# Kernel tuning notes

Measured on AMD Instinct MI355X. Metric: run time of the kernel, lower is better.

The kernel has to match this reference:

```python
import jax, jax.numpy as jnp
import numpy as np

B, N, D = 8, 1024, 768
H = 12
HD = D // H
LN_EPS = 1e-5
EPS = 1e-8


def setup_inputs() -> dict:
    key = jax.random.key(0)
    ks = jax.random.split(key, 16)
    s = 0.02
    return {
        "x": jax.random.normal(ks[0], (B, N, D), jnp.float32),
        "low_freq_feat": jax.random.normal(ks[1], (B, N, D), jnp.float32),
        "high_freq_feat": jax.random.normal(ks[2], (B, N, D), jnp.float32),
        "W_qkv_id": jax.random.normal(ks[3], (D, 3 * D), jnp.float32) * s,
        "W_qkv_attr": jax.random.normal(ks[4], (D, 3 * D), jnp.float32) * s,
        "W_fg_id": jax.random.normal(ks[5], (D, D), jnp.float32) * s,
        "b_fg_id": jnp.zeros((D,), jnp.float32),
        "W_fg_attr": jax.random.normal(ks[6], (D, D), jnp.float32) * s,
        "b_fg_attr": jnp.zeros((D,), jnp.float32),
        "W_proj_id": jax.random.normal(ks[7], (D, D), jnp.float32) * s,
        "b_proj_id": jnp.zeros((D,), jnp.float32),
        "W_proj_attr": jax.random.normal(ks[8], (D, D), jnp.float32) * s,
        "b_proj_attr": jnp.zeros((D,), jnp.float32),
        "ln_id_g": jnp.ones((D,), jnp.float32),
        "ln_id_b": jnp.zeros((D,), jnp.float32),
        "ln_attr_g": jnp.ones((D,), jnp.float32),
        "ln_attr_b": jnp.zeros((D,), jnp.float32),
        "ortho_temperature": jnp.float32(1.0),
        "freq_guide_strength": jnp.float32(0.3),
    }


def _layernorm(x, g, b):
    mu = x.mean(-1, keepdims=True)
    var = ((x - mu) ** 2).mean(-1, keepdims=True)
    return (x - mu) * jax.lax.rsqrt(var + LN_EPS) * g + b


def reference(x, low_freq_feat, high_freq_feat,
              W_qkv_id, W_qkv_attr,
              W_fg_id, b_fg_id, W_fg_attr, b_fg_attr,
              W_proj_id, b_proj_id, W_proj_attr, b_proj_attr,
              ln_id_g, ln_id_b, ln_attr_g, ln_attr_b,
              ortho_temperature, freq_guide_strength):
    b, n, d = x.shape
    scale = HD ** -0.5

    def split_qkv(t):
        t = t.reshape(b, n, 3, H, HD).transpose(2, 0, 3, 1, 4)
        return t[0], t[1], t[2]

    q_id, k_id, v_id = split_qkv(x @ W_qkv_id)
    q_at, k_at, v_at = split_qkv(x @ W_qkv_attr)

    fs = jax.nn.sigmoid(freq_guide_strength)
    low_g = (low_freq_feat @ W_fg_id + b_fg_id).reshape(b, n, H, HD).transpose(0, 2, 1, 3)
    high_g = (high_freq_feat @ W_fg_attr + b_fg_attr).reshape(b, n, H, HD).transpose(0, 2, 1, 3)
    v_id = v_id + fs * low_g
    v_at = v_at + fs * high_g

    def soft_attn(q, k):
        a = jnp.clip(jnp.einsum('bhnd,bhmd->bhnm', q, k) * scale, -20.0, 20.0)
        return jax.nn.softmax(a, axis=-1)

    attn_id = soft_attn(q_id, k_id)
    attn_at = soft_attn(q_at, k_at)

    # soft orthogonal mask (same mask for both branches)
    overlap = ((attn_id + EPS) * (attn_at + EPS)).sum(-1, keepdims=True)
    temp = jnp.clip(ortho_temperature, 0.1, 5.0)
    mask = jax.nn.sigmoid(-overlap * temp)

    def mask_renorm(a):
        m = a * mask
        m = m / (m.sum(-1, keepdims=True) + EPS)
        return jnp.where(jnp.isnan(m), jnp.zeros_like(m), m)

    attn_id = mask_renorm(attn_id)
    attn_at = mask_renorm(attn_at)

    def branch_out(a, v, W, bias, g, beta):
        o = jnp.einsum('bhnm,bhmd->bhnd', a, v).transpose(0, 2, 1, 3).reshape(b, n, d)
        return _layernorm(o @ W + bias, g, beta)

    id_features = branch_out(attn_id, v_id, W_proj_id, b_proj_id, ln_id_g, ln_id_b)
    attr_features = branch_out(attn_at, v_at, W_proj_attr, b_proj_attr, ln_attr_g, ln_attr_b)
    return (id_features, attr_features)
```

## Files before the change

kernel.cpp:

```cpp
#include <hip/hip_runtime.h>
#include <stdint.h>


typedef __attribute__((ext_vector_type(8))) _Float16 f16x8;
typedef __attribute__((ext_vector_type(4))) _Float16 f16x4;
typedef __attribute__((ext_vector_type(4))) float    f32x4;

__device__ __forceinline__ void g2l16(const void* g, void* l) {
  __builtin_amdgcn_global_load_lds(
      (const __attribute__((address_space(1))) void*)g,
      (__attribute__((address_space(3))) void*)l, 16, 0, 0);
}

#define BARX()   asm volatile("s_barrier" ::: "memory")
#define WAITV(N) asm volatile("s_waitcnt vmcnt(" #N ")" ::: "memory")

template <bool SWAP>
__device__ __forceinline__ void gemm256(const _Float16* __restrict__ A,
                                        const _Float16* __restrict__ Bt,
                                        int K, int m0, int n0,
                                        _Float16* As, _Float16* Bs,
                                        f32x4 (&acc)[8][4]) {
  const int tid = threadIdx.x;
  const int lane = tid & 63, w = tid >> 6;
  const int wm = (w >> 2) * 128, wn = (w & 3) * 64;
  const int l15 = lane & 15, quad = lane >> 4;
  const int srow = lane >> 2;
  const int scol = ((lane & 3) ^ ((lane >> 3) & 3)) * 8;
  const int rg = (quad ^ ((l15 >> 1) & 3)) * 8;
  const int c0 = w * 2, c1 = c0 + 1;
  const _Float16* pA0 = A + (m0 + c0 * 16 + srow) * K + scol;
  const _Float16* pA1 = A + (m0 + c1 * 16 + srow) * K + scol;
  const _Float16* pB0 = Bt + (n0 + c0 * 16 + srow) * K + scol;
  const _Float16* pB1 = Bt + (n0 + c1 * 16 + srow) * K + scol;

#pragma unroll
  for (int mt = 0; mt < 8; mt++)
#pragma unroll
    for (int nt = 0; nt < 4; nt++) acc[mt][nt] = (f32x4){0.f, 0.f, 0.f, 0.f};

  const int KT = K >> 5;

#pragma unroll
  for (int t = 0; t < 3; t++) {
    int kc = t * 32, bj = t * 8192;
    g2l16(pA0 + kc, As + bj + c0 * 512);
    g2l16(pB0 + kc, Bs + bj + c0 * 512);
    g2l16(pA1 + kc, As + bj + c1 * 512);
    g2l16(pB1 + kc, Bs + bj + c1 * 512);
  }
  WAITV(8);
  BARX();

  auto tile = [&](int t, bool doStage) {
    const int bj = (t & 3) * 8192;
    const _Float16* as = As + bj;
    const _Float16* bs = Bs + bj;
    const int kcn = (t + 3) * 32;
    const int bn = ((t + 3) & 3) * 8192;
    f16x8 a[8];
#pragma unroll
    for (int mt = 0; mt < 8; mt++)
      a[mt] = *(const f16x8*)(as + (wm + mt * 16 + l15) * 32 + rg);
    f16x8 b0 = *(const f16x8*)(bs + (wn + l15) * 32 + rg);
    f16x8 b1 = *(const f16x8*)(bs + (wn + 16 + l15) * 32 + rg);
    if (doStage) {
      g2l16(pA0 + kcn, As + bn + c0 * 512);
      g2l16(pA1 + kcn, As + bn + c1 * 512);
    }
    __builtin_amdgcn_s_setprio(1);
#pragma unroll
    for (int mt = 0; mt < 8; mt++) {
      acc[mt][0] = SWAP
          ? __builtin_amdgcn_mfma_f32_16x16x32_f16(b0, a[mt], acc[mt][0], 0, 0, 0)
          : __builtin_amdgcn_mfma_f32_16x16x32_f16(a[mt], b0, acc[mt][0], 0, 0, 0);
      acc[mt][1] = SWAP
          ? __builtin_amdgcn_mfma_f32_16x16x32_f16(b1, a[mt], acc[mt][1], 0, 0, 0)
          : __builtin_amdgcn_mfma_f32_16x16x32_f16(a[mt], b1, acc[mt][1], 0, 0, 0);
    }
    __builtin_amdgcn_s_setprio(0);
    BARX();
    f16x8 b2 = *(const f16x8*)(bs + (wn + 32 + l15) * 32 + rg);
    f16x8 b3 = *(const f16x8*)(bs + (wn + 48 + l15) * 32 + rg);
    if (doStage) {
      g2l16(pB0 + kcn, Bs + bn + c0 * 512);
      g2l16(pB1 + kcn, Bs + bn + c1 * 512);
    }
    __builtin_amdgcn_s_setprio(1);
#pragma unroll
    for (int mt = 0; mt < 8; mt++) {
      acc[mt][2] = SWAP
          ? __builtin_amdgcn_mfma_f32_16x16x32_f16(b2, a[mt], acc[mt][2], 0, 0, 0)
          : __builtin_amdgcn_mfma_f32_16x16x32_f16(a[mt], b2, acc[mt][2], 0, 0, 0);
      acc[mt][3] = SWAP
          ? __builtin_amdgcn_mfma_f32_16x16x32_f16(b3, a[mt], acc[mt][3], 0, 0, 0)
          : __builtin_amdgcn_mfma_f32_16x16x32_f16(a[mt], b3, acc[mt][3], 0, 0, 0);
    }
    __builtin_amdgcn_s_setprio(0);
  };

  int t = 0;
  for (; t < KT - 3; ++t) {
    tile(t, true);
    WAITV(8);
    BARX();
  }
  tile(t, false); WAITV(4); BARX(); ++t;
  tile(t, false); WAITV(0); BARX(); ++t;
  tile(t, false);
}

__global__ __launch_bounds__(256) void k_cast3(const float* __restrict__ s0,
                                               const float* __restrict__ s1,
                                               const float* __restrict__ s2,
                                               _Float16* __restrict__ d0,
                                               _Float16* __restrict__ d1,
                                               _Float16* __restrict__ d2) {
  int blk = blockIdx.x;
  const float* s; _Float16* d;
  if (blk < 6144)       { s = s0; d = d0; }
  else if (blk < 12288) { s = s1; d = d1; blk -= 6144; }
  else                  { s = s2; d = d2; blk -= 12288; }
  int i = blk * 256 + threadIdx.x;
  float4 v = ((const float4*)s)[i];
  f16x4 o = {(_Float16)v.x, (_Float16)v.y, (_Float16)v.z, (_Float16)v.w};
  *(f16x4*)(d + (size_t)i * 4) = o;
}

__device__ __forceinline__ void tcast32(const float* __restrict__ src,
                                        _Float16* __restrict__ dst,
                                        int N, int n0, int k0) {
  __shared__ float t[32][33];
  int tr = threadIdx.x >> 5, tc = threadIdx.x & 31;
#pragma unroll
  for (int i = 0; i < 4; i++) {
    int r = tr + i * 8;
    t[r][tc] = src[(size_t)(k0 + r) * N + n0 + tc];
  }
  __syncthreads();
#pragma unroll
  for (int i = 0; i < 4; i++) {
    int r = tr + i * 8;
    dst[(size_t)(n0 + r) * 768 + k0 + tc] = (_Float16)t[tc][r];
  }
}

__global__ __launch_bounds__(256) void k_tcast_all(const float* __restrict__ Wq0,
                                                   const float* __restrict__ Wq1,
                                                   const float* __restrict__ W0,
                                                   const float* __restrict__ W1,
                                                   const float* __restrict__ W2,
                                                   const float* __restrict__ W3,
                                                   _Float16* __restrict__ Dq,
                                                   _Float16* __restrict__ D0,
                                                   _Float16* __restrict__ D1,
                                                   _Float16* __restrict__ D2,
                                                   _Float16* __restrict__ D3) {
  int blk = blockIdx.x;
  if (blk < 3456) {
    int half = blk / 1728, rem = blk % 1728;
    int xx = rem % 72, yy = rem / 72;
    tcast32(half ? Wq1 : Wq0, Dq + (size_t)half * 2304 * 768, 2304, xx * 32, yy * 32);
  } else {
    blk -= 3456;
    int q = blk / 576, rem = blk % 576;
    int xx = rem % 24, yy = rem / 24;
    const float* src; _Float16* d;
    if (q == 0)      { src = W0; d = D0; }
    else if (q == 1) { src = W1; d = D1; }
    else if (q == 2) { src = W2; d = D2; }
    else             { src = W3; d = D3; }
    tcast32(src, d, 768, xx * 32, yy * 32);
  }
}

__global__ __launch_bounds__(512, 2) void k_gemm_qkv(const _Float16* __restrict__ A,
                                                     const _Float16* __restrict__ Bt,
                                                     _Float16* __restrict__ Qb,
                                                     _Float16* __restrict__ Kb,
                                                     _Float16* __restrict__ Vtb) {
  __shared__ alignas(16) _Float16 As[32768], Bs[32768];
  f32x4 acc[8][4];
  int m0 = blockIdx.y * 256, n0 = blockIdx.x * 256;
  int br = n0 / 2304;
  int three = (n0 - br * 2304) / 768;
  int lane = threadIdx.x & 63, w = threadIdx.x >> 6;
  int wm = (w >> 2) * 128, wn = (w & 3) * 64, l15 = lane & 15, quad = lane >> 4;

  if (three == 2) {
    gemm256<false>(A, Bt, 768, m0, n0, As, Bs, acc);
#pragma unroll
    for (int mt = 0; mt < 8; mt++)
#pragma unroll
      for (int nt = 0; nt < 4; nt++) {
        int n = n0 + wn + nt * 16 + l15;
        int c = n - br * 2304 - 1536;
        int h = c >> 6, hd = c & 63;
        int m = m0 + wm + mt * 16 + quad * 4;
        int b = m >> 10, tok = m & 1023;
        size_t head = (size_t)(br * 96 + b * 12 + h);
        f32x4 v = acc[mt][nt];
        f16x4 o;
#pragma unroll
        for (int r = 0; r < 4; r++) o[r] = (_Float16)v[r];
        *(f16x4*)(Vtb + (head * 64 + hd) * 1024 + tok) = o;
      }
  } else {
    gemm256<true>(A, Bt, 768, m0, n0, As, Bs, acc);
    float qscl = (three == 0) ? 0.125f * 1.44269504f : 1.0f;
    _Float16* dst = (three == 0) ? Qb : Kb;
#pragma unroll
    for (int mt = 0; mt < 8; mt++)
#pragma unroll
      for (int nt = 0; nt < 4; nt++) {
        int m = m0 + wm + mt * 16 + l15;
        int n = n0 + wn + nt * 16 + quad * 4;
        int c = n - br * 2304 - three * 768;
        int h = c >> 6, hd = c & 63;
        int b = m >> 10, tok = m & 1023;
        size_t head = (size_t)(br * 96 + b * 12 + h);
        f32x4 v = acc[mt][nt];
        f16x4 o;
#pragma unroll
        for (int r = 0; r < 4; r++) o[r] = (_Float16)(v[r] * qscl);
        *(f16x4*)(dst + (head * 1024 + tok) * 64 + hd) = o;
      }
  }
}

__global__ __launch_bounds__(512, 2) void k_gemm_fgadd(const _Float16* __restrict__ Alo,
                                                       const _Float16* __restrict__ Ahi,
                                                       const _Float16* __restrict__ Bid,
                                                       const _Float16* __restrict__ Bat,
                                                       const float* __restrict__ bid,
                                                       const float* __restrict__ bat,
                                                       const float* __restrict__ fgs,
                                                       _Float16* __restrict__ Vtb) {
  __shared__ alignas(16) _Float16 As[32768], Bs[32768];
  f32x4 acc[8][4];
  int br = blockIdx.x / 3;
  int n0 = (blockIdx.x % 3) * 256, m0 = blockIdx.y * 256;
  const _Float16* A = br ? Ahi : Alo;
  const _Float16* Bt = br ? Bat : Bid;
  const float* bias = br ? bat : bid;
  gemm256<false>(A, Bt, 768, m0, n0, As, Bs, acc);
  float fs = 1.f / (1.f + __expf(-fgs[0]));
  int lane = threadIdx.x & 63, w = threadIdx.x >> 6;
  int wm = (w >> 2) * 128, wn = (w & 3) * 64, l15 = lane & 15, quad = lane >> 4;
#pragma unroll
  for (int mt = 0; mt < 8; mt++)
#pragma unroll
    for (int nt = 0; nt < 4; nt++) {
      int c = n0 + wn + nt * 16 + l15;
      int h = c >> 6, hd = c & 63;
      int m = m0 + wm + mt * 16 + quad * 4;
      int b = m >> 10, tok = m & 1023;
      size_t head = (size_t)(br * 96 + b * 12 + h);
      float bv = bias[c];
      f32x4 v = acc[mt][nt];
      _Float16* p = Vtb + (head * 64 + hd) * 1024 + tok;
      f16x4 old = *(const f16x4*)p;
      f16x4 o;
#pragma unroll
      for (int r = 0; r < 4; r++)
        o[r] = (_Float16)((float)old[r] + fs * (v[r] + bv));
      *(f16x4*)p = o;
    }
}

__global__ __launch_bounds__(256, 3) void k_attn(const _Float16* __restrict__ Qb,
                                                 const _Float16* __restrict__ Kb,
                                                 const _Float16* __restrict__ Vtb,
                                                 _Float16* __restrict__ Ob) {
  __shared__ alignas(16) _Float16 Qs[128 * 64];
  __shared__ alignas(16) _Float16 Ks[128 * 64];
  __shared__ alignas(16) _Float16 Vts[64 * 128];
  int hl = blockIdx.x;
  int br = hl / 96, bh = hl % 96;
  int qbase = blockIdx.y * 128;
  const _Float16* Qh = Qb + (size_t)hl * 65536;
  const _Float16* Kh = Kb + (size_t)hl * 65536;
  const _Float16* Vth = Vtb + (size_t)hl * 65536;
  int lane = threadIdx.x & 63, w = threadIdx.x >> 6;
  int l15 = lane & 15, quad = lane >> 4;
  const int key7 = l15 & 7;

  {
    int rr = lane >> 3, sg = (lane & 7) ^ rr;
#pragma unroll
    for (int i = 0; i < 4; i++) {
      int c = w * 4 + i;
      g2l16(Qh + (size_t)(qbase + c * 8 + rr) * 64 + sg * 8, Qs + c * 512);
    }
  }
  auto stage_kv = [&](int n0) {
    int rr8 = lane >> 3, sg8 = ((lane & 7) ^ rr8) * 8;
    int rr16 = lane >> 4;
#pragma unroll
    for (int i = 0; i < 4; i++) {
      int c = w * 4 + i;
      g2l16(Kh + (size_t)(n0 + c * 8 + rr8) * 64 + sg8, Ks + c * 512);
      int vrow = c * 4 + rr16;
      int sg16 = ((lane & 15) ^ (vrow & 15)) * 8;
      g2l16(Vth + (size_t)vrow * 1024 + n0 + sg16, Vts + c * 512);
    }
  };
  stage_kv(0);

  f32x4 o[2][4];
#pragma unroll
  for (int qg = 0; qg < 2; qg++)
#pragma unroll
    for (int i = 0; i < 4; i++) o[qg][i] = (f32x4){0.f, 0.f, 0.f, 0.f};
  float rs0 = 0.f, rs1 = 0.f;
  f16x8 bq[2][2];
  const f32x4 zero = (f32x4){0.f, 0.f, 0.f, 0.f};
  const int g0 = (quad ^ key7) * 8, g1 = ((4 + quad) ^ key7) * 8;

  for (int kt = 0; kt < 8; kt++) {
    __syncthreads();
    if (kt == 0) {
#pragma unroll
      for (int qg = 0; qg < 2; qg++) {
        bq[qg][0] = *(const f16x8*)(Qs + (w * 32 + qg * 16 + l15) * 64 + g0);
        bq[qg][1] = *(const f16x8*)(Qs + (w * 32 + qg * 16 + l15) * 64 + g1);
      }
    }
    f32x4 c0, c1;
    {
      f16x8 a0 = *(const f16x8*)(Ks + l15 * 64 + g0);
      f16x8 a1 = *(const f16x8*)(Ks + l15 * 64 + g1);
      c0 = __builtin_amdgcn_mfma_f32_16x16x32_f16(a0, bq[0][0], zero, 0, 0, 0);
      c0 = __builtin_amdgcn_mfma_f32_16x16x32_f16(a1, bq[0][1], c0, 0, 0, 0);
      c1 = __builtin_amdgcn_mfma_f32_16x16x32_f16(a0, bq[1][0], zero, 0, 0, 0);
      c1 = __builtin_amdgcn_mfma_f32_16x16x32_f16(a1, bq[1][1], c1, 0, 0, 0);
    }
#pragma unroll
    for (int nt = 0; nt < 8; nt++) {
      f32x4 n0_, n1_;
      if (nt < 7) {
        f16x8 a0 = *(const f16x8*)(Ks + ((nt + 1) * 16 + l15) * 64 + g0);
        f16x8 a1 = *(const f16x8*)(Ks + ((nt + 1) * 16 + l15) * 64 + g1);
        n0_ = __builtin_amdgcn_mfma_f32_16x16x32_f16(a0, bq[0][0], zero, 0, 0, 0);
        n0_ = __builtin_amdgcn_mfma_f32_16x16x32_f16(a1, bq[0][1], n0_, 0, 0, 0);
        n1_ = __builtin_amdgcn_mfma_f32_16x16x32_f16(a0, bq[1][0], zero, 0, 0, 0);
        n1_ = __builtin_amdgcn_mfma_f32_16x16x32_f16(a1, bq[1][1], n1_, 0, 0, 0);
      }
      f16x4 pt0, pt1;
#pragma unroll
      for (int r = 0; r < 4; r++) {
        float p = __builtin_amdgcn_exp2f(c0[r]);
        rs0 += p; pt0[r] = (_Float16)p;
      }
#pragma unroll
      for (int r = 0; r < 4; r++) {
        float p = __builtin_amdgcn_exp2f(c1[r]);
        rs1 += p; pt1[r] = (_Float16)p;
      }
#pragma unroll
      for (int hdt = 0; hdt < 4; hdt++) {
        int g = ((2 * nt + (quad >> 1)) ^ l15) * 8 + (quad & 1) * 4;
        f16x4 av = *(const f16x4*)(Vts + (hdt * 16 + l15) * 128 + g);
        o[0][hdt] = __builtin_amdgcn_mfma_f32_16x16x16f16(av, pt0, o[0][hdt], 0, 0, 0);
        o[1][hdt] = __builtin_amdgcn_mfma_f32_16x16x16f16(av, pt1, o[1][hdt], 0, 0, 0);
      }
      if (nt < 7) { c0 = n0_; c1 = n1_; }
    }
    __syncthreads();
    if (kt < 7) stage_kv((kt + 1) * 128);
  }
  int b = bh / 12, h = bh % 12;
#pragma unroll
  for (int qg = 0; qg < 2; qg++) {
    float l = qg ? rs1 : rs0;
    l += __shfl_xor(l, 16);
    l += __shfl_xor(l, 32);
    float inv = 1.f / l;
    size_t rowb = ((size_t)br * 8192 + b * 1024 + qbase + w * 32 + qg * 16 + l15) * 768 +
                  h * 64;
#pragma unroll
    for (int hdt = 0; hdt < 4; hdt++) {
      f16x4 u;
#pragma unroll
      for (int r = 0; r < 4; r++) u[r] = (_Float16)(o[qg][hdt][r] * inv);
      *(f16x4*)(Ob + rowb + hdt * 16 + quad * 4) = u;
    }
  }
}

__global__ __launch_bounds__(512, 2) void k_gemm_proj2(const _Float16* __restrict__ Aid,
                                                       const _Float16* __restrict__ Aat,
                                                       const _Float16* __restrict__ Bid,
                                                       const _Float16* __restrict__ Bat,
                                                       _Float16* __restrict__ Yid,
                                                       _Float16* __restrict__ Yat) {
  __shared__ alignas(16) _Float16 As[32768], Bs[32768];
  f32x4 acc[8][4];
  int half = blockIdx.x / 3;
  int n0 = (blockIdx.x % 3) * 256, m0 = blockIdx.y * 256;
  const _Float16* A = half ? Aat : Aid;
  const _Float16* Bt = half ? Bat : Bid;
  _Float16* Y = half ? Yat : Yid;
  gemm256<true>(A, Bt, 768, m0, n0, As, Bs, acc);
  int lane = threadIdx.x & 63, w = threadIdx.x >> 6;
  int wm = (w >> 2) * 128, wn = (w & 3) * 64, l15 = lane & 15, quad = lane >> 4;
#pragma unroll
  for (int mt = 0; mt < 8; mt++)
#pragma unroll
    for (int nt = 0; nt < 4; nt++) {
      int m = m0 + wm + mt * 16 + l15;
      int n = n0 + wn + nt * 16 + quad * 4;
      f32x4 v = acc[mt][nt];
      f16x4 o;
#pragma unroll
      for (int r = 0; r < 4; r++) o[r] = (_Float16)v[r];
      *(f16x4*)(Y + (size_t)m * 768 + n) = o;
    }
}

__global__ __launch_bounds__(256) void k_ln(const _Float16* __restrict__ Yid,
                                            const _Float16* __restrict__ Yat,
                                            const float* __restrict__ bp_id,
                                            const float* __restrict__ bp_at,
                                            const float* __restrict__ g_id,
                                            const float* __restrict__ be_id,
                                            const float* __restrict__ g_at,
                                            const float* __restrict__ be_at,
                                            float* __restrict__ out) {
  int w = threadIdx.x >> 6, lane = threadIdx.x & 63;
  int r = blockIdx.x * 4 + w;
  int br = r >> 13, m = r & 8191;
  const _Float16* Y = br ? Yat : Yid;
  const float* bp = br ? bp_at : bp_id;
  const float* g = br ? g_at : g_id;
  const float* be = br ? be_at : be_id;
  float v[12], sum = 0.f, sq = 0.f;
#pragma unroll
  for (int j = 0; j < 3; j++) {
    int c = j * 256 + lane * 4;
    f16x4 y = *(const f16x4*)(Y + (size_t)m * 768 + c);
    float4 bv = *(const float4*)(bp + c);
#pragma unroll
    for (int r2 = 0; r2 < 4; r2++) {
      float t = (float)y[r2] + ((const float*)&bv)[r2];
      v[j * 4 + r2] = t; sum += t; sq += t * t;
    }
  }
#pragma unroll
  for (int d = 1; d < 64; d <<= 1) { sum += __shfl_xor(sum, d); sq += __shfl_xor(sq, d); }
  float mu = sum * (1.f / 768.f);
  float var = sq * (1.f / 768.f) - mu * mu;
  float rstd = rsqrtf(var + 1e-5f);
  float* op = out + (size_t)br * 6291456 + (size_t)m * 768;
#pragma unroll
  for (int j = 0; j < 3; j++) {
    int c = j * 256 + lane * 4;
    float4 gv = *(const float4*)(g + c);
    float4 bev = *(const float4*)(be + c);
    float4 ov;
#pragma unroll
    for (int r2 = 0; r2 < 4; r2++)
      ((float*)&ov)[r2] = (v[j * 4 + r2] - mu) * rstd * ((const float*)&gv)[r2] +
                          ((const float*)&bev)[r2];
    *(float4*)(op + c) = ov;
  }
}

extern "C" void kernel_launch(void* const* d_in, const int* in_sizes, int n_in,
                              void* d_out, int out_size, void* d_ws, size_t ws_size,
                              hipStream_t stream) {
  const float* x       = (const float*)d_in[0];
  const float* lowf    = (const float*)d_in[1];
  const float* highf   = (const float*)d_in[2];
  const float* Wqkv_id = (const float*)d_in[3];
  const float* Wqkv_at = (const float*)d_in[4];
  const float* Wfg_id  = (const float*)d_in[5];
  const float* bfg_id  = (const float*)d_in[6];
  const float* Wfg_at  = (const float*)d_in[7];
  const float* bfg_at  = (const float*)d_in[8];
  const float* Wpr_id  = (const float*)d_in[9];
  const float* bpr_id  = (const float*)d_in[10];
  const float* Wpr_at  = (const float*)d_in[11];
  const float* bpr_at  = (const float*)d_in[12];
  const float* g_id    = (const float*)d_in[13];
  const float* be_id   = (const float*)d_in[14];
  const float* g_at    = (const float*)d_in[15];
  const float* be_at   = (const float*)d_in[16];
  const float* fgs     = (const float*)d_in[18];

  char* ws = (char*)d_ws;
  _Float16* x_f    = (_Float16*)(ws + 0);
  _Float16* low_f  = (_Float16*)(ws + 12582912);
  _Float16* high_f = (_Float16*)(ws + 25165824);
  _Float16* wqkvt  = (_Float16*)(ws + 37748736);
  _Float16* wfgidt = (_Float16*)(ws + 44826624);
  _Float16* wfgatt = (_Float16*)(ws + 46006272);
  _Float16* wpridt = (_Float16*)(ws + 47185920);
  _Float16* wpratt = (_Float16*)(ws + 48365568);
  _Float16* Qb     = (_Float16*)(ws + 74711040);
  _Float16* Kb     = (_Float16*)(ws + 99876864);
  _Float16* Vtb    = (_Float16*)(ws + 125042688);
  _Float16* Ob     = (_Float16*)(ws + 150208512);
  _Float16* Y_id   = (_Float16*)(ws + 0);
  _Float16* Y_at   = (_Float16*)(ws + 49545216);

  k_cast3<<<18432, 256, 0, stream>>>(x, lowf, highf, x_f, low_f, high_f);
  k_tcast_all<<<5760, 256, 0, stream>>>(Wqkv_id, Wqkv_at, Wfg_id, Wfg_at, Wpr_id, Wpr_at,
                                        wqkvt, wfgidt, wfgatt, wpridt, wpratt);
  k_gemm_qkv<<<dim3(18, 32), 512, 0, stream>>>(x_f, wqkvt, Qb, Kb, Vtb);
  k_gemm_fgadd<<<dim3(6, 32), 512, 0, stream>>>(low_f, high_f, wfgidt, wfgatt,
                                                bfg_id, bfg_at, fgs, Vtb);
  k_attn<<<dim3(192, 8), 256, 0, stream>>>(Qb, Kb, Vtb, Ob);
  k_gemm_proj2<<<dim3(6, 32), 512, 0, stream>>>(Ob, Ob + 6291456, wpridt, wpratt,
                                                Y_id, Y_at);
  k_ln<<<4096, 256, 0, stream>>>(Y_id, Y_at, bpr_id, bpr_at, g_id, be_id, g_at, be_at,
                                 (float*)d_out);
}
```

Before: 410.3 us.

## Reshape GEMM warp tiling to 64x128 per wave with explicit barrier scheduling

Changes the per-wave output tile in the shared 256x256 GEMM from 128x64 to 64x128, so each wave loads 4 A fragments and 8 B fragments per k-step instead of 8 and 4. The main loop is rewritten as a single loop with explicit barriers, lgkmcnt waits and sched_barriers between the two MFMA halves. The goal is to balance LDS reads and control instruction interleaving in the QKV, frequency-guide and projection GEMMs. The extra barriers per k-step add synchronization cost, and the epilogues are updated to the new accumulator layout.

```diff
diff --git a/kernel.cpp b/kernel.cpp
--- a/kernel.cpp
+++ b/kernel.cpp
@@ -14,100 +14,95 @@
 
 #define BARX()   asm volatile("s_barrier" ::: "memory")
 #define WAITV(N) asm volatile("s_waitcnt vmcnt(" #N ")" ::: "memory")
+#define LGKM0()  asm volatile("s_waitcnt lgkmcnt(0)" ::: "memory")
+#define SB0()    __builtin_amdgcn_sched_barrier(0)
+
+#define MFMA16(NB)                                                             \
+  __builtin_amdgcn_s_setprio(1);                                               \
+  _Pragma("unroll")                                                            \
+  for (int mt = 0; mt < 4; mt++)                                               \
+    _Pragma("unroll")                                                          \
+    for (int i = 0; i < 4; i++)                                                \
+      acc[mt][(NB) + i] = SWAP                                                 \
+          ? __builtin_amdgcn_mfma_f32_16x16x32_f16(b[(NB) + i], a[mt],         \
+                                                   acc[mt][(NB) + i], 0, 0, 0) \
+          : __builtin_amdgcn_mfma_f32_16x16x32_f16(a[mt], b[(NB) + i],         \
+                                                   acc[mt][(NB) + i], 0, 0, 0);\
+  __builtin_amdgcn_s_setprio(0);
 
 template <bool SWAP>
 __device__ __forceinline__ void gemm256(const _Float16* __restrict__ A,
                                         const _Float16* __restrict__ Bt,
                                         int K, int m0, int n0,
                                         _Float16* As, _Float16* Bs,
-                                        f32x4 (&acc)[8][4]) {
+                                        f32x4 (&acc)[4][8]) {
   const int tid = threadIdx.x;
   const int lane = tid & 63, w = tid >> 6;
-  const int wm = (w >> 2) * 128, wn = (w & 3) * 64;
+  const int wm = (w >> 1) * 64, wn = (w & 1) * 128;
   const int l15 = lane & 15, quad = lane >> 4;
   const int srow = lane >> 2;
   const int scol = ((lane & 3) ^ ((lane >> 3) & 3)) * 8;
   const int rg = (quad ^ ((l15 >> 1) & 3)) * 8;
-  const int c0 = w * 2, c1 = c0 + 1;
-  const _Float16* pA0 = A + (m0 + c0 * 16 + srow) * K + scol;
-  const _Float16* pA1 = A + (m0 + c1 * 16 + srow) * K + scol;
-  const _Float16* pB0 = Bt + (n0 + c0 * 16 + srow) * K + scol;
-  const _Float16* pB1 = Bt + (n0 + c1 * 16 + srow) * K + scol;
-
-#pragma unroll
-  for (int mt = 0; mt < 8; mt++)
-#pragma unroll
-    for (int nt = 0; nt < 4; nt++) acc[mt][nt] = (f32x4){0.f, 0.f, 0.f, 0.f};
-
+  const int rdA = (wm + l15) * 32 + rg;
+  const int rdB = (wn + l15) * 32 + rg;
   const int KT = K >> 5;
 
-#pragma unroll
-  for (int t = 0; t < 3; t++) {
-    int kc = t * 32, bj = t * 8192;
-    g2l16(pA0 + kc, As + bj + c0 * 512);
-    g2l16(pB0 + kc, Bs + bj + c0 * 512);
-    g2l16(pA1 + kc, As + bj + c1 * 512);
-    g2l16(pB1 + kc, Bs + bj + c1 * 512);
-  }
+  const _Float16* gA0 = A + (size_t)(m0 + (w * 2) * 16 + srow) * K + scol;
+  const _Float16* gA1 = gA0 + (size_t)16 * K;
+  const _Float16* gB0 = Bt + (size_t)(n0 + (w * 2) * 16 + srow) * K + scol;
+  const _Float16* gB1 = gB0 + (size_t)16 * K;
+
+  auto stageA = [&](int t) {
+    _Float16* Ab = As + (t & 3) * 8192 + w * 1024;
+    const int kc = t * 32;
+    g2l16(gA0 + kc, Ab);
+    g2l16(gA1 + kc, Ab + 512);
+  };
+  auto stageB = [&](int t) {
+    _Float16* Bb = Bs + (t & 3) * 8192 + w * 1024;
+    const int kc = t * 32;
+    g2l16(gB0 + kc, Bb);
+    g2l16(gB1 + kc, Bb + 512);
+  };
+
+#pragma unroll
+  for (int mt = 0; mt < 4; mt++)
+#pragma unroll
+    for (int nt = 0; nt < 8; nt++) acc[mt][nt] = (f32x4){0.f, 0.f, 0.f, 0.f};
+
+  stageA(0); stageB(0);
+  stageA(1); stageB(1);
+  stageA(2); stageB(2);
   WAITV(8);
   BARX();
 
-  auto tile = [&](int t, bool doStage) {
-    const int bj = (t & 3) * 8192;
-    const _Float16* as = As + bj;
-    const _Float16* bs = Bs + bj;
-    const int kcn = (t + 3) * 32;
-    const int bn = ((t + 3) & 3) * 8192;
-    f16x8 a[8];
-#pragma unroll
-    for (int mt = 0; mt < 8; mt++)
-      a[mt] = *(const f16x8*)(as + (wm + mt * 16 + l15) * 32 + rg);
-    f16x8 b0 = *(const f16x8*)(bs + (wn + l15) * 32 + rg);
-    f16x8 b1 = *(const f16x8*)(bs + (wn + 16 + l15) * 32 + rg);
-    if (doStage) {
-      g2l16(pA0 + kcn, As + bn + c0 * 512);
-      g2l16(pA1 + kcn, As + bn + c1 * 512);
-    }
-    __builtin_amdgcn_s_setprio(1);
-#pragma unroll
-    for (int mt = 0; mt < 8; mt++) {
-      acc[mt][0] = SWAP
-          ? __builtin_amdgcn_mfma_f32_16x16x32_f16(b0, a[mt], acc[mt][0], 0, 0, 0)
-          : __builtin_amdgcn_mfma_f32_16x16x32_f16(a[mt], b0, acc[mt][0], 0, 0, 0);
-      acc[mt][1] = SWAP
-          ? __builtin_amdgcn_mfma_f32_16x16x32_f16(b1, a[mt], acc[mt][1], 0, 0, 0)
-          : __builtin_amdgcn_mfma_f32_16x16x32_f16(a[mt], b1, acc[mt][1], 0, 0, 0);
-    }
-    __builtin_amdgcn_s_setprio(0);
+  for (int t = 0; t < KT; t++) {
+    const _Float16* as = As + (t & 3) * 8192;
+    const _Float16* bs = Bs + (t & 3) * 8192;
+    const bool st = (t + 3 < KT);
+    f16x8 a[4], b[8];
+
+#pragma unroll
+    for (int mt = 0; mt < 4; mt++) a[mt] = *(const f16x8*)(as + rdA + mt * 512);
+#pragma unroll
+    for (int i = 0; i < 4; i++) b[i] = *(const f16x8*)(bs + rdB + i * 512);
+    if (st) stageA(t + 3);
+    BARX(); LGKM0(); SB0();
+    MFMA16(0);
+    SB0();
     BARX();
-    f16x8 b2 = *(const f16x8*)(bs + (wn + 32 + l15) * 32 + rg);
-    f16x8 b3 = *(const f16x8*)(bs + (wn + 48 + l15) * 32 + rg);
-    if (doStage) {
-      g2l16(pB0 + kcn, Bs + bn + c0 * 512);
-      g2l16(pB1 + kcn, Bs + bn + c1 * 512);
-    }
-    __builtin_amdgcn_s_setprio(1);
-#pragma unroll
-    for (int mt = 0; mt < 8; mt++) {
-      acc[mt][2] = SWAP
-          ? __builtin_amdgcn_mfma_f32_16x16x32_f16(b2, a[mt], acc[mt][2], 0, 0, 0)
-          : __builtin_amdgcn_mfma_f32_16x16x32_f16(a[mt], b2, acc[mt][2], 0, 0, 0);
-      acc[mt][3] = SWAP
-          ? __builtin_amdgcn_mfma_f32_16x16x32_f16(b3, a[mt], acc[mt][3], 0, 0, 0)
-          : __builtin_amdgcn_mfma_f32_16x16x32_f16(a[mt], b3, acc[mt][3], 0, 0, 0);
-    }
-    __builtin_amdgcn_s_setprio(0);
-  };
-
-  int t = 0;
-  for (; t < KT - 3; ++t) {
-    tile(t, true);
-    WAITV(8);
-    BARX();
-  }
-  tile(t, false); WAITV(4); BARX(); ++t;
-  tile(t, false); WAITV(0); BARX(); ++t;
-  tile(t, false);
+
+#pragma unroll
+    for (int i = 4; i < 8; i++) b[i] = *(const f16x8*)(bs + rdB + i * 512);
+    if (st) stageB(t + 3);
+    BARX(); LGKM0(); SB0();
+    MFMA16(4);
+    SB0();
+    if (t + 3 < KT)      { WAITV(8); }
+    else if (t + 2 < KT) { WAITV(4); }
+    else if (t + 1 < KT) { WAITV(0); }
+    if (t + 1 < KT) BARX();
+  }
 }
 
 __global__ __launch_bounds__(256) void k_cast3(const float* __restrict__ s0,
@@ -180,19 +175,19 @@
                                                      _Float16* __restrict__ Kb,
                                                      _Float16* __restrict__ Vtb) {
   __shared__ alignas(16) _Float16 As[32768], Bs[32768];
-  f32x4 acc[8][4];
+  f32x4 acc[4][8];
   int m0 = blockIdx.y * 256, n0 = blockIdx.x * 256;
   int br = n0 / 2304;
   int three = (n0 - br * 2304) / 768;
   int lane = threadIdx.x & 63, w = threadIdx.x >> 6;
-  int wm = (w >> 2) * 128, wn = (w & 3) * 64, l15 = lane & 15, quad = lane >> 4;
+  int wm = (w >> 1) * 64, wn = (w & 1) * 128, l15 = lane & 15, quad = lane >> 4;
 
   if (three == 2) {
     gemm256<false>(A, Bt, 768, m0, n0, As, Bs, acc);
 #pragma unroll
-    for (int mt = 0; mt < 8; mt++)
-#pragma unroll
-      for (int nt = 0; nt < 4; nt++) {
+    for (int mt = 0; mt < 4; mt++)
+#pragma unroll
+      for (int nt = 0; nt < 8; nt++) {
         int n = n0 + wn + nt * 16 + l15;
         int c = n - br * 2304 - 1536;
         int h = c >> 6, hd = c & 63;
@@ -210,9 +205,9 @@
     float qscl = (three == 0) ? 0.125f * 1.44269504f : 1.0f;
     _Float16* dst = (three == 0) ? Qb : Kb;
 #pragma unroll
-    for (int mt = 0; mt < 8; mt++)
-#pragma unroll
-      for (int nt = 0; nt < 4; nt++) {
+    for (int mt = 0; mt < 4; mt++)
+#pragma unroll
+      for (int nt = 0; nt < 8; nt++) {
         int m = m0 + wm + mt * 16 + l15;
         int n = n0 + wn + nt * 16 + quad * 4;
         int c = n - br * 2304 - three * 768;
@@ -237,7 +232,7 @@
                                                        const float* __restrict__ fgs,
                                                        _Float16* __restrict__ Vtb) {
   __shared__ alignas(16) _Float16 As[32768], Bs[32768];
-  f32x4 acc[8][4];
+  f32x4 acc[4][8];
   int br = blockIdx.x / 3;
   int n0 = (blockIdx.x % 3) * 256, m0 = blockIdx.y * 256;
   const _Float16* A = br ? Ahi : Alo;
@@ -246,11 +241,11 @@
   gemm256<false>(A, Bt, 768, m0, n0, As, Bs, acc);
   float fs = 1.f / (1.f + __expf(-fgs[0]));
   int lane = threadIdx.x & 63, w = threadIdx.x >> 6;
-  int wm = (w >> 2) * 128, wn = (w & 3) * 64, l15 = lane & 15, quad = lane >> 4;
-#pragma unroll
-  for (int mt = 0; mt < 8; mt++)
-#pragma unroll
-    for (int nt = 0; nt < 4; nt++) {
+  int wm = (w >> 1) * 64, wn = (w & 1) * 128, l15 = lane & 15, quad = lane >> 4;
+#pragma unroll
+  for (int mt = 0; mt < 4; mt++)
+#pragma unroll
+    for (int nt = 0; nt < 8; nt++) {
       int c = n0 + wn + nt * 16 + l15;
       int h = c >> 6, hd = c & 63;
       int m = m0 + wm + mt * 16 + quad * 4;
@@ -395,7 +390,7 @@
                                                        _Float16* __restrict__ Yid,
                                                        _Float16* __restrict__ Yat) {
   __shared__ alignas(16) _Float16 As[32768], Bs[32768];
-  f32x4 acc[8][4];
+  f32x4 acc[4][8];
   int half = blockIdx.x / 3;
   int n0 = (blockIdx.x % 3) * 256, m0 = blockIdx.y * 256;
   const _Float16* A = half ? Aat : Aid;
@@ -403,11 +398,11 @@
   _Float16* Y = half ? Yat : Yid;
   gemm256<true>(A, Bt, 768, m0, n0, As, Bs, acc);
   int lane = threadIdx.x & 63, w = threadIdx.x >> 6;
-  int wm = (w >> 2) * 128, wn = (w & 3) * 64, l15 = lane & 15, quad = lane >> 4;
-#pragma unroll
-  for (int mt = 0; mt < 8; mt++)
-#pragma unroll
-    for (int nt = 0; nt < 4; nt++) {
+  int wm = (w >> 1) * 64, wn = (w & 1) * 128, l15 = lane & 15, quad = lane >> 4;
+#pragma unroll
+  for (int mt = 0; mt < 4; mt++)
+#pragma unroll
+    for (int nt = 0; nt < 8; nt++) {
       int m = m0 + wm + mt * 16 + l15;
       int n = n0 + wn + nt * 16 + quad * 4;
       f32x4 v = acc[mt][nt];
```

After: 431.3 us. 5.1% more time.
